# Performance work log

Measured on AMD Instinct MI355X. Metric: run time of the kernel, lower is better.

The kernel has to match this reference:

```python
import jax, jax.numpy as jnp
import numpy as np
from jax import lax

B, NPG, IN, OUT, ETYPES, STEPS, E = 16, 1024, 128, 256, 2, 6, 262144
N = B * NPG
CONCAT = IN + OUT
EPS = 1e-5


def setup_inputs() -> dict:
    key = jax.random.key(0)
    ks = jax.random.split(key, 24)
    s = 0.05
    return {
        "features": jax.random.normal(ks[0], (N, IN), jnp.float32),
        "src": jax.random.randint(ks[1], (E,), 0, N, jnp.int32),
        "dst": jax.random.randint(ks[2], (E,), 0, N, jnp.int32),
        "etype": jax.random.randint(ks[3], (E,), 0, ETYPES, jnp.int32),
        # GGNN per-etype linears (weight, bias) and GRUCell params
        "W_lin": jax.random.normal(ks[4], (ETYPES, OUT, OUT), jnp.float32) * s,
        "b_lin": jnp.zeros((ETYPES, OUT), jnp.float32),
        "W_ih": jax.random.normal(ks[5], (3 * OUT, OUT), jnp.float32) * s,
        "W_hh": jax.random.normal(ks[6], (3 * OUT, OUT), jnp.float32) * s,
        "b_ih": jnp.zeros((3 * OUT,), jnp.float32),
        "b_hh": jnp.zeros((3 * OUT,), jnp.float32),
        # conv branch on h_i (OUT channels)
        "conv1_w": jax.random.normal(ks[7], (OUT, OUT, 3), jnp.float32) * s,
        "conv1_b": jnp.zeros((OUT,), jnp.float32),
        "conv2_w": jax.random.normal(ks[8], (OUT, OUT, 1), jnp.float32) * s,
        "conv2_b": jnp.zeros((OUT,), jnp.float32),
        # conv branch on c_i (CONCAT channels)
        "convc1_w": jax.random.normal(ks[9], (CONCAT, CONCAT, 3), jnp.float32) * s,
        "convc1_b": jnp.zeros((CONCAT,), jnp.float32),
        "convc2_w": jax.random.normal(ks[10], (CONCAT, CONCAT, 1), jnp.float32) * s,
        "convc2_b": jnp.zeros((CONCAT,), jnp.float32),
        # shared batchnorms (training-mode batch stats, affine params)
        "bn_g": jnp.ones((OUT,), jnp.float32),
        "bn_b": jnp.zeros((OUT,), jnp.float32),
        "bnc_g": jnp.ones((CONCAT,), jnp.float32),
        "bnc_b": jnp.zeros((CONCAT,), jnp.float32),
        # gating MLPs
        "mlpy_w": jax.random.normal(ks[11], (2, OUT), jnp.float32) * s,
        "mlpy_b": jnp.zeros((2,), jnp.float32),
        "mlpz_w": jax.random.normal(ks[12], (2, CONCAT), jnp.float32) * s,
        "mlpz_b": jnp.zeros((2,), jnp.float32),
    }


def _bn_relu(x, g, b):  # x: [B, C, L], training-mode BN (biased var)
    mean = x.mean(axis=(0, 2), keepdims=True)
    var = ((x - mean) ** 2).mean(axis=(0, 2), keepdims=True)
    xn = (x - mean) * lax.rsqrt(var + EPS)
    return jax.nn.relu(xn * g[None, :, None] + b[None, :, None])


def _conv1d(x, w, b):  # x: [B, C, L], w: [O, I, K]
    y = lax.conv_general_dilated(x, w, (1,), 'VALID',
                                 dimension_numbers=('NCH', 'OIH', 'NCH'))
    return y + b[None, :, None]


def _maxpool(x, k, s):
    return lax.reduce_window(x, -jnp.inf, lax.max, (1, 1, k), (1, 1, s), 'VALID')


def _forward(features, src, dst, etype, W_lin, b_lin, W_ih, W_hh, b_ih, b_hh,
             conv1_w, conv1_b, conv2_w, conv2_b, convc1_w, convc1_b,
             convc2_w, convc2_b, bn_g, bn_b, bnc_g, bnc_b,
             mlpy_w, mlpy_b, mlpz_w, mlpz_b):
    # --- GatedGraphConv (DGL semantics): pad, n_steps of msg-pass + GRUCell ---
    h = jnp.pad(features, ((0, 0), (0, OUT - IN)))  # [N, OUT]
    for _ in range(STEPS):
        # per-etype linear applied to all nodes: [ETYPES, N, OUT]
        Wh = jnp.einsum('nd,ekd->enk', h, W_lin) + b_lin[:, None, :]
        msg = Wh[etype, src]                              # [E, OUT] gather
        agg = jax.ops.segment_sum(msg, dst, num_segments=N)  # scatter-add
        gi = agg @ W_ih.T + b_ih
        gh = h @ W_hh.T + b_hh
        ir, iz, ig = jnp.split(gi, 3, axis=-1)
        hr, hz, hg = jnp.split(gh, 3, axis=-1)
        r = jax.nn.sigmoid(ir + hr)
        z = jax.nn.sigmoid(iz + hz)
        n = jnp.tanh(ig + r * hg)
        h = (1.0 - z) * n + z * h

    h_i = h.reshape(B, NPG, OUT)
    x_i = features.reshape(B, NPG, IN)
    c_i = jnp.concatenate([h_i, x_i], axis=-1)  # [B, NPG, CONCAT]

    hT = jnp.swapaxes(h_i, 1, 2)  # [B, OUT, NPG]
    Y1 = _maxpool(_bn_relu(_conv1d(hT, conv1_w, conv1_b), bn_g, bn_b), 3, 2)
    Y2 = jnp.swapaxes(_maxpool(_bn_relu(_conv1d(Y1, conv2_w, conv2_b), bn_g, bn_b), 2, 2), 1, 2)

    cT = jnp.swapaxes(c_i, 1, 2)  # [B, CONCAT, NPG]
    Z1 = _maxpool(_bn_relu(_conv1d(cT, convc1_w, convc1_b), bnc_g, bnc_b), 3, 2)
    Z2 = jnp.swapaxes(_maxpool(_bn_relu(_conv1d(Z1, convc2_w, convc2_b), bnc_g, bnc_b), 2, 2), 1, 2)

    before_avg = (Y2 @ mlpy_w.T + mlpy_b) * (Z2 @ mlpz_w.T + mlpz_b)  # [B, L, 2]
    return jax.nn.sigmoid(before_avg.mean(axis=1))  # [B, 2]


def reference(features, src, dst, etype, W_lin, b_lin, W_ih, W_hh, b_ih, b_hh,
              conv1_w, conv1_b, conv2_w, conv2_b, convc1_w, convc1_b,
              convc2_w, convc2_b, bn_g, bn_b, bnc_g, bnc_b,
              mlpy_w, mlpy_b, mlpz_w, mlpz_b):
    return _forward(features, src, dst, etype, W_lin, b_lin, W_ih, W_hh, b_ih, b_hh,
                    conv1_w, conv1_b, conv2_w, conv2_b, convc1_w, convc1_b,
                    convc2_w, convc2_b, bn_g, bn_b, bnc_g, bnc_b,
                    mlpy_w, mlpy_b, mlpz_w, mlpz_b)
```

## Files before the change

kernel.cpp:

```cpp
#include <hip/hip_runtime.h>
#include <math.h>

constexpr int Bn     = 16;
constexpr int NPG    = 1024;
constexpr int Nn     = Bn * NPG;
constexpr int FIN    = 128;
constexpr int FOUT   = 256;
constexpr int CCAT   = 384;
constexpr int STEPS  = 6;
constexpr int NE     = 262144;

using short8 = __attribute__((ext_vector_type(8))) short;
using f32x4  = __attribute__((ext_vector_type(4))) float;

static __device__ __forceinline__ unsigned short f2bf(float x) {
    union { float f; unsigned u; } v; v.f = x;
    unsigned r = (v.u + 0x7FFFu + ((v.u >> 16) & 1u)) >> 16;
    return (unsigned short)r;
}
static __device__ __forceinline__ float bf2f(unsigned short b) {
    union { unsigned u; float f; } v; v.u = ((unsigned)b) << 16;
    return v.f;
}
static __device__ __forceinline__ float sigm(float x) { return 1.f / (1.f + expf(-x)); }

static __device__ __forceinline__ void gload16(const void* g, void* l) {
    __builtin_amdgcn_global_load_lds(
        (const __attribute__((address_space(1))) void*)g,
        (__attribute__((address_space(3))) void*)l, 16, 0, 0);
}


__global__ void cvt_bf(const float* __restrict__ s, unsigned short* __restrict__ d, int n) {
    int i = blockIdx.x * 256 + threadIdx.x;
    if (i < n) d[i] = f2bf(s[i]);
}

__global__ void cvt_wcat(const float* __restrict__ Wih, const float* __restrict__ Whh,
                         unsigned short* __restrict__ Wcat) {
    int o = blockIdx.x * 256 + threadIdx.x;
    int k = o >> 9, j = o & 511;
    float v = (j < 256) ? Whh[(size_t)k * 256 + j] : Wih[(size_t)k * 256 + (j - 256)];
    Wcat[o] = f2bf(v);
}

__global__ void add_bias(const float* __restrict__ a, const float* __restrict__ b,
                         float* __restrict__ o, int n) {
    int i = blockIdx.x * 256 + threadIdx.x;
    if (i < n) o[i] = a[i] + b[i];
}

__global__ void cvt_wconv(const float* __restrict__ W, unsigned short* __restrict__ Wt,
                          int C, int KW, int n) {
    int o = blockIdx.x * 256 + threadIdx.x;
    if (o >= n) return;
    int c = o / (KW * C), rem = o % (KW * C);
    int kb = rem / C, i = rem % C;
    Wt[o] = f2bf(W[(size_t)(c * C + i) * KW + kb]);
}

__global__ void pad_h(const float* __restrict__ f, float* __restrict__ h,
                      unsigned short* __restrict__ Acat) {
    int i = blockIdx.x * 256 + threadIdx.x;
    int k = i & 255, n = i >> 8;
    float v = (k < FIN) ? f[(size_t)n * FIN + k] : 0.f;
    h[i] = v; Acat[(size_t)n * 512 + k] = f2bf(v);
}

__global__ void build_cb(const unsigned short* __restrict__ Acat, const float* __restrict__ f,
                         unsigned short* __restrict__ cb) {
    int idx = blockIdx.x * 256 + threadIdx.x;
    int c = idx % CCAT, n = idx / CCAT;
    cb[idx] = (c < FOUT) ? Acat[(size_t)n * 512 + c] : f2bf(f[(size_t)n * FIN + (c - FOUT)]);
}


__global__ void edge_count(const int* __restrict__ dst, int* __restrict__ deg) {
    int e = blockIdx.x * 256 + threadIdx.x;
    atomicAdd(&deg[dst[e]], 1);
}

__global__ __launch_bounds__(1024) void scan_deg(const int* __restrict__ deg,
                                                 int* __restrict__ rowptr,
                                                 int* __restrict__ cursor) {
    __shared__ int ps[1024];
    const int t = threadIdx.x;
    int loc[16]; int s = 0;
    const int base = t * 16;
#pragma unroll
    for (int i = 0; i < 16; ++i) { loc[i] = deg[base + i]; s += loc[i]; }
    ps[t] = s;
    __syncthreads();
    for (int off = 1; off < 1024; off <<= 1) {
        int add = (t >= off) ? ps[t - off] : 0;
        __syncthreads();
        ps[t] += add;
        __syncthreads();
    }
    int run = ps[t] - s;
#pragma unroll
    for (int i = 0; i < 16; ++i) { rowptr[base + i] = run; cursor[base + i] = run; run += loc[i]; }
    if (t == 1023) rowptr[16384] = run;
}

__global__ void edge_fill(const int* __restrict__ src, const int* __restrict__ dst,
                          const int* __restrict__ et, int* __restrict__ cursor,
                          int* __restrict__ widx) {
    int e = blockIdx.x * 256 + threadIdx.x;
    int slot = atomicAdd(&cursor[dst[e]], 1);
    widx[slot] = src[e] * 2 + et[e];
}

static __device__ __forceinline__ void gemm128_body(
    const unsigned short* __restrict__ Ab, const unsigned short* __restrict__ W,
    const float* __restrict__ bias, float* __restrict__ Cf,
    unsigned short* __restrict__ Cb, int Ctap, int lda, int L, int Lv, int N, int K,
    int outBf, int l0, int col0, unsigned short* As, unsigned short* Bs) {
    const int t = threadIdx.x;
    const int w = t >> 6, l = t & 63;
    const int lr = l & 15, lhi = l >> 4;
    const int wr = w >> 1, wc = w & 1;
    const int srow8 = l >> 3;
    const int scole = ((l & 7) ^ srow8) * 8;
    const int lx7 = l & 7;

    f32x4 acc[4][4] = {};

    for (int k0 = 0; k0 < K; k0 += 64) {
        const int kb = k0 / Ctap;
        const int i0 = k0 - kb * Ctap;
        __syncthreads();
#pragma unroll
        for (int p = 0; p < 4; ++p) {
            const int r = w * 32 + p * 8;
            int srow = l0 + r + srow8 + kb;
            srow = srow < L ? srow : L - 1;
            gload16(Ab + (size_t)srow * lda + i0 + scole, &As[r * 64]);
            gload16(W + (size_t)(col0 + r + srow8) * K + k0 + scole, &Bs[r * 64]);
        }
        __syncthreads();
        const int abase = (wr * 64 + lr) * 64;
        const int bbase = (wc * 64 + lr) * 64;
#pragma unroll
        for (int kk = 0; kk < 2; ++kk) {
            const int soff = ((kk * 4 + lhi) ^ lx7) * 8;
            short8 af[4], bw[4];
#pragma unroll
            for (int fi = 0; fi < 4; ++fi)
                af[fi] = *(const short8*)&As[abase + fi * 1024 + soff];
#pragma unroll
            for (int fj = 0; fj < 4; ++fj)
                bw[fj] = *(const short8*)&Bs[bbase + fj * 1024 + soff];
#pragma unroll
            for (int fi = 0; fi < 4; ++fi)
#pragma unroll
                for (int fj = 0; fj < 4; ++fj)
                    acc[fi][fj] = __builtin_amdgcn_mfma_f32_16x16x32_bf16(
                        af[fi], bw[fj], acc[fi][fj], 0, 0, 0);
        }
    }
    const int rb = lhi * 4;
#pragma unroll
    for (int fi = 0; fi < 4; ++fi)
#pragma unroll
        for (int fj = 0; fj < 4; ++fj) {
            const int gcol = col0 + wc * 64 + fj * 16 + lr;
            const float bv = bias[gcol];
#pragma unroll
            for (int rr = 0; rr < 4; ++rr) {
                const int grow = l0 + wr * 64 + fi * 16 + rb + rr;
                if (grow < Lv) {
                    float v = acc[fi][fj][rr] + bv;
                    const size_t o = (size_t)grow * N + gcol;
                    if (outBf) Cb[o] = f2bf(v);
                    else       Cf[o] = v;
                }
            }
        }
}

__global__ __launch_bounds__(256) void gemm128_swz(
    const unsigned short* __restrict__ A, const unsigned short* __restrict__ W,
    const float* __restrict__ bias, unsigned short* __restrict__ Cb,
    int lda, int N, int K) {
    __shared__ unsigned short As[128 * 64];
    __shared__ unsigned short Bs[128 * 64];
    const int gX = gridDim.x;
    const int hId = blockIdx.x + gX * blockIdx.y;
    const int xcd = hId & 7, tt = hId >> 3;
    const int bx = tt % gX, by = xcd + 8 * (tt / gX);
    gemm128_body(A, W, bias, nullptr, Cb, lda, lda, Nn, Nn, N, K, 1,
                 by * 128, bx * 128, As, Bs);
}

__global__ __launch_bounds__(256) void gemm128_pair2(
    const unsigned short* __restrict__ A1, const unsigned short* __restrict__ W1,
    const float* __restrict__ b1, float* __restrict__ C1,
    int Ctap1, int lda1, int L1, int Lv1, int N1, int K1, int nx1, int ny1,
    const unsigned short* __restrict__ A2, const unsigned short* __restrict__ W2,
    const float* __restrict__ b2, float* __restrict__ C2,
    int Ctap2, int lda2, int L2, int Lv2, int N2, int K2, int nx2, int ny2) {
    __shared__ unsigned short As[128 * 64];
    __shared__ unsigned short Bs[128 * 64];
    int id = blockIdx.x;
    const int n1 = nx1 * ny1 * Bn;
    if (id < n1) {
        int x = id % nx1, y = (id / nx1) % ny1, z = id / (nx1 * ny1);
        gemm128_body(A1 + (size_t)z * L1 * lda1, W1, b1,
                     C1 + (size_t)z * Lv1 * N1, nullptr,
                     Ctap1, lda1, L1, Lv1, N1, K1, 0, y * 128, x * 128, As, Bs);
    } else {
        id -= n1;
        int x = id % nx2, y = (id / nx2) % ny2, z = id / (nx2 * ny2);
        gemm128_body(A2 + (size_t)z * L2 * lda2, W2, b2,
                     C2 + (size_t)z * Lv2 * N2, nullptr,
                     Ctap2, lda2, L2, Lv2, N2, K2, 0, y * 128, x * 128, As, Bs);
    }
}

__global__ __launch_bounds__(256) void gemm_gru(
    const unsigned short* __restrict__ Acat, const unsigned short* __restrict__ Wcat,
    const unsigned short* __restrict__ Whg, const float* __restrict__ bias_s,
    const float* __restrict__ bias_g, float* __restrict__ h,
    unsigned short* __restrict__ Anext) {
    __shared__ unsigned short As[64 * 64];
    __shared__ unsigned short Bs[256 * 64];
    const int hId = blockIdx.x + 4 * blockIdx.y;
    const int xcd = hId & 7, tt = hId >> 3;
    const int bx = tt & 3, by = xcd + 8 * (tt >> 2);
    const int l0 = by * 64, c0 = bx * 64;

    const int t = threadIdx.x;
    const int w = t >> 6, l = t & 63;
    const int lr = l & 15, lhi = l >> 4;
    const int srow8 = l >> 3;
    const int scole = ((l & 7) ^ srow8) * 8;
    const int lx7 = l & 7;

    f32x4 acc[16] = {};

#pragma unroll
    for (int k0 = 0; k0 < 512; k0 += 64) {
        __syncthreads();
#pragma unroll
        for (int p = 0; p < 2; ++p) {
            const int r = w * 16 + p * 8;
            gload16(Acat + (size_t)(l0 + r + srow8) * 512 + k0 + scole, &As[r * 64]);
        }
#pragma unroll
        for (int p = 0; p < 8; ++p) {
            const int r = w * 64 + p * 8;
            if (r < 192) {
                const int g = r >> 6;
                const int cr = (r & 63) + srow8;
                gload16(Wcat + (size_t)(g * 256 + c0 + cr) * 512 + k0 + scole, &Bs[r * 64]);
            } else if (k0 < 256) {
                const int cr = (r - 192) + srow8;
                gload16(Whg + (size_t)(c0 + cr) * 256 + k0 + scole, &Bs[r * 64]);
            }
        }
        __syncthreads();
        const int abase = (w * 16 + lr) * 64;
#pragma unroll
        for (int kk = 0; kk < 2; ++kk) {
            const int soff = ((kk * 4 + lhi) ^ lx7) * 8;
            short8 a0 = *(const short8*)&As[abase + soff];
#pragma unroll
            for (int g = 0; g < 4; ++g) {
                if (!(g == 3 && k0 >= 256)) {
#pragma unroll
                    for (int fj = 0; fj < 4; ++fj) {
                        short8 bb = *(const short8*)&Bs[(g * 64 + fj * 16 + lr) * 64 + soff];
                        acc[g * 4 + fj] = __builtin_amdgcn_mfma_f32_16x16x32_bf16(
                            a0, bb, acc[g * 4 + fj], 0, 0, 0);
                    }
                }
            }
        }
    }
    const int rb = lhi * 4;
#pragma unroll
    for (int fj = 0; fj < 4; ++fj) {
        const int c = c0 + fj * 16 + lr;
        const float br = bias_s[c];
        const float bz = bias_s[256 + c];
        const float bg = bias_s[512 + c];
        const float bh = bias_g[c];
#pragma unroll
        for (int rr = 0; rr < 4; ++rr) {
            const int grow = l0 + w * 16 + rb + rr;
            float sr = acc[0 * 4 + fj][rr] + br;
            float sz = acc[1 * 4 + fj][rr] + bz;
            float sg = acc[2 * 4 + fj][rr] + bg;
            float hg = acc[3 * 4 + fj][rr] + bh;
            float r = sigm(sr), z = sigm(sz);
            float nn = tanhf(sg - (1.f - r) * hg);
            const size_t ho = (size_t)grow * 256 + c;
            float hv = (1.f - z) * nn + z * h[ho];
            h[ho] = hv;
            Anext[(size_t)grow * 512 + c] = f2bf(hv);
        }
    }
}

__global__ __launch_bounds__(64) void gather_agg(
    const unsigned short* __restrict__ Whb, const int* __restrict__ rowptr,
    const int* __restrict__ widx, unsigned short* __restrict__ Acat) {
    const int n = blockIdx.x, t = threadIdx.x;
    const int s0 = rowptr[n], s1 = rowptr[n + 1];
    float p0[4] = {}, p1[4] = {}, p2[4] = {}, p3[4] = {};
    int s = s0;
    for (; s + 4 <= s1; s += 4) {
        const int w0 = widx[s], w1 = widx[s + 1], w2 = widx[s + 2], w3 = widx[s + 3];
        const ushort4 v0 = *(const ushort4*)(Whb + (size_t)w0 * 256 + t * 4);
        const ushort4 v1 = *(const ushort4*)(Whb + (size_t)w1 * 256 + t * 4);
        const ushort4 v2 = *(const ushort4*)(Whb + (size_t)w2 * 256 + t * 4);
        const ushort4 v3 = *(const ushort4*)(Whb + (size_t)w3 * 256 + t * 4);
        p0[0] += bf2f(v0.x); p0[1] += bf2f(v0.y); p0[2] += bf2f(v0.z); p0[3] += bf2f(v0.w);
        p1[0] += bf2f(v1.x); p1[1] += bf2f(v1.y); p1[2] += bf2f(v1.z); p1[3] += bf2f(v1.w);
        p2[0] += bf2f(v2.x); p2[1] += bf2f(v2.y); p2[2] += bf2f(v2.z); p2[3] += bf2f(v2.w);
        p3[0] += bf2f(v3.x); p3[1] += bf2f(v3.y); p3[2] += bf2f(v3.z); p3[3] += bf2f(v3.w);
    }
    for (; s < s1; ++s) {
        const int wi = widx[s];
        const ushort4 v = *(const ushort4*)(Whb + (size_t)wi * 256 + t * 4);
        p0[0] += bf2f(v.x); p0[1] += bf2f(v.y); p0[2] += bf2f(v.z); p0[3] += bf2f(v.w);
    }
    ushort4 o;
    o.x = f2bf(p0[0] + p1[0] + p2[0] + p3[0]);
    o.y = f2bf(p0[1] + p1[1] + p2[1] + p3[1]);
    o.z = f2bf(p0[2] + p1[2] + p2[2] + p3[2]);
    o.w = f2bf(p0[3] + p1[3] + p2[3] + p3[3]);
    *(ushort4*)(Acat + (size_t)n * 512 + 256 + t * 4) = o;
}

constexpr int NCHUNK = 128;

static __device__ __forceinline__ void bn_part_body(
    const float* __restrict__ X, float* __restrict__ pS, float* __restrict__ pQ,
    int C, int totalRows, int rowsPerChunk, int bx, int by) {
    const int t  = threadIdx.x;
    const int cq = t & 31, rl = t >> 5;
    const int c0 = bx * 128 + cq * 4;
    const int r0 = by * rowsPerChunk;
    const int r1 = min(r0 + rowsPerChunk, totalRows);
    float s0 = 0, s1 = 0, s2 = 0, s3 = 0, q0 = 0, q1 = 0, q2 = 0, q3 = 0;
    for (int r = r0 + rl; r < r1; r += 8) {
        float4 v = *(const float4*)(X + (size_t)r * C + c0);
        s0 += v.x; s1 += v.y; s2 += v.z; s3 += v.w;
        q0 += v.x * v.x; q1 += v.y * v.y; q2 += v.z * v.z; q3 += v.w * v.w;
    }
    __shared__ float ls[8][128], lq[8][128];
    ls[rl][cq * 4 + 0] = s0; ls[rl][cq * 4 + 1] = s1;
    ls[rl][cq * 4 + 2] = s2; ls[rl][cq * 4 + 3] = s3;
    lq[rl][cq * 4 + 0] = q0; lq[rl][cq * 4 + 1] = q1;
    lq[rl][cq * 4 + 2] = q2; lq[rl][cq * 4 + 3] = q3;
    __syncthreads();
    if (rl == 0) {
#pragma unroll
        for (int i = 0; i < 4; ++i) {
            const int c = cq * 4 + i;
            float ss = 0, qq = 0;
#pragma unroll
            for (int j = 0; j < 8; ++j) { ss += ls[j][c]; qq += lq[j][c]; }
            pS[(size_t)by * C + c0 + i] = ss;
            pQ[(size_t)by * C + c0 + i] = qq;
        }
    }
}

__global__ __launch_bounds__(256) void bn_part_pair(
    const float* __restrict__ X1, float* __restrict__ pS1, float* __restrict__ pQ1, int C1,
    const float* __restrict__ X2, float* __restrict__ pS2, float* __restrict__ pQ2, int C2,
    int totalRows, int rowsPerChunk) {
    int id = blockIdx.x;
    const int n1 = (C1 / 128) * NCHUNK;
    if (id < n1)
        bn_part_body(X1, pS1, pQ1, C1, totalRows, rowsPerChunk, id % (C1 / 128), id / (C1 / 128));
    else {
        id -= n1;
        bn_part_body(X2, pS2, pQ2, C2, totalRows, rowsPerChunk, id % (C2 / 128), id / (C2 / 128));
    }
}

__global__ __launch_bounds__(128) void bn_reduce_pair(
    const float* __restrict__ pS1, const float* __restrict__ pQ1,
    float* __restrict__ mean1, float* __restrict__ var1, int C1,
    const float* __restrict__ pS2, const float* __restrict__ pQ2,
    float* __restrict__ mean2, float* __restrict__ var2, int C2, int totalRows) {
    int c = blockIdx.x;
    const float* pS; const float* pQ; float* mean; float* var; int C;
    if (c < C1) { pS = pS1; pQ = pQ1; mean = mean1; var = var1; C = C1; }
    else { c -= C1; pS = pS2; pQ = pQ2; mean = mean2; var = var2; C = C2; }
    const int t = threadIdx.x;
    __shared__ float rs[128], rq[128];
    rs[t] = pS[(size_t)t * C + c];
    rq[t] = pQ[(size_t)t * C + c];
    __syncthreads();
    for (int st = 64; st; st >>= 1) {
        if (t < st) { rs[t] += rs[t + st]; rq[t] += rq[t + st]; }
        __syncthreads();
    }
    if (t == 0) {
        float m = rs[0] / totalRows;
        mean[c] = m;
        var[c]  = rq[0] / totalRows - m * m;
    }
}

static __device__ __forceinline__ void bnp_body(
    const float* __restrict__ X, const float* __restrict__ mean,
    const float* __restrict__ var, const float* __restrict__ g,
    const float* __restrict__ bta, float* __restrict__ Of,
    unsigned short* __restrict__ Ob, int C, int Lin, int Lout, int Kp, int outBf, int idx) {
    if (idx >= Bn * Lout * C) return;
    int c = idx % C, j = (idx / C) % Lout, b = idx / (C * Lout);
    float sc = g[c] * rsqrtf(var[c] + 1e-5f);
    float sh = bta[c] - mean[c] * sc;
    const float* xb = X + ((size_t)b * Lin + j * 2) * C + c;
    float m = 0.f;
    for (int k = 0; k < Kp; ++k) m = fmaxf(m, xb[(size_t)k * C] * sc + sh);
    if (outBf) Ob[idx] = f2bf(m);
    else       Of[idx] = m;
}

__global__ void bnp_pair(
    const float* __restrict__ X1, const float* __restrict__ mean1,
    const float* __restrict__ var1, const float* __restrict__ g1,
    const float* __restrict__ b1, float* __restrict__ Of1,
    unsigned short* __restrict__ Ob1, int C1,
    const float* __restrict__ X2, const float* __restrict__ mean2,
    const float* __restrict__ var2, const float* __restrict__ g2,
    const float* __restrict__ b2, float* __restrict__ Of2,
    unsigned short* __restrict__ Ob2, int C2,
    int Lin, int Lout, int Kp, int outBf) {
    int id = blockIdx.x;
    const int nb1 = (Bn * Lout * C1 + 255) / 256;
    if (id < nb1)
        bnp_body(X1, mean1, var1, g1, b1, Of1, Ob1, C1, Lin, Lout, Kp, outBf,
                 id * 256 + threadIdx.x);
    else
        bnp_body(X2, mean2, var2, g2, b2, Of2, Ob2, C2, Lin, Lout, Kp, outBf,
                 (id - nb1) * 256 + threadIdx.x);
}

__global__ void final_dot(const float* __restrict__ Y2, const float* __restrict__ Z2,
                          const float* __restrict__ wy, const float* __restrict__ by,
                          const float* __restrict__ wz, const float* __restrict__ bz,
                          float* __restrict__ prod) {
    const int b = blockIdx.y, j = blockIdx.x, t = threadIdx.x;
    float p0 = 0, p1 = 0, q0 = 0, q1 = 0;
    const float* yrow = Y2 + (size_t)(b * 255 + j) * FOUT;
    const float* zrow = Z2 + (size_t)(b * 255 + j) * CCAT;
    for (int c = t; c < FOUT; c += 128) {
        float v = yrow[c];
        p0 += v * wy[c]; p1 += v * wy[FOUT + c];
    }
    for (int c = t; c < CCAT; c += 128) {
        float v = zrow[c];
        q0 += v * wz[c]; q1 += v * wz[CCAT + c];
    }
    __shared__ float r0[128], r1[128], r2[128], r3[128];
    r0[t] = p0; r1[t] = p1; r2[t] = q0; r3[t] = q1;
    __syncthreads();
    for (int s = 64; s; s >>= 1) {
        if (t < s) { r0[t] += r0[t + s]; r1[t] += r1[t + s]; r2[t] += r2[t + s]; r3[t] += r3[t + s]; }
        __syncthreads();
    }
    if (t == 0) {
        float y0 = r0[0] + by[0], y1 = r1[0] + by[1];
        float z0 = r2[0] + bz[0], z1 = r3[0] + bz[1];
        prod[((size_t)b * 255 + j) * 2 + 0] = y0 * z0;
        prod[((size_t)b * 255 + j) * 2 + 1] = y1 * z1;
    }
}

__global__ void final_out(const float* __restrict__ prod, float* __restrict__ out) {
    const int b = blockIdx.x, t = threadIdx.x;
    const int w = t >> 6, lane = t & 63;
    float s = 0.f;
    for (int j = lane; j < 255; j += 64) s += prod[((size_t)b * 255 + j) * 2 + w];
#pragma unroll
    for (int off = 32; off; off >>= 1) s += __shfl_down(s, off);
    if (lane == 0) out[b * 2 + w] = 1.f / (1.f + expf(-s / 255.f));
}

extern "C" void kernel_launch(void* const* d_in, const int* in_sizes, int n_in,
                              void* d_out, int out_size, void* d_ws, size_t ws_size,
                              hipStream_t stream) {
    (void)in_sizes; (void)n_in; (void)out_size; (void)ws_size;
    const float* features = (const float*)d_in[0];
    const int*   src      = (const int*)d_in[1];
    const int*   dst      = (const int*)d_in[2];
    const int*   etype    = (const int*)d_in[3];
    const float* W_lin    = (const float*)d_in[4];
    const float* b_lin    = (const float*)d_in[5];
    const float* W_ih     = (const float*)d_in[6];
    const float* W_hh     = (const float*)d_in[7];
    const float* b_ih     = (const float*)d_in[8];
    const float* b_hh     = (const float*)d_in[9];
    const float* conv1_w  = (const float*)d_in[10];
    const float* conv1_b  = (const float*)d_in[11];
    const float* conv2_w  = (const float*)d_in[12];
    const float* conv2_b  = (const float*)d_in[13];
    const float* convc1_w = (const float*)d_in[14];
    const float* convc1_b = (const float*)d_in[15];
    const float* convc2_w = (const float*)d_in[16];
    const float* convc2_b = (const float*)d_in[17];
    const float* bn_g     = (const float*)d_in[18];
    const float* bn_b     = (const float*)d_in[19];
    const float* bnc_g    = (const float*)d_in[20];
    const float* bnc_b    = (const float*)d_in[21];
    const float* mlpy_w   = (const float*)d_in[22];
    const float* mlpy_b   = (const float*)d_in[23];
    const float* mlpz_w   = (const float*)d_in[24];
    const float* mlpz_b   = (const float*)d_in[25];

    float* ws = (float*)d_ws;
    float*          h      = ws;
    unsigned short* Acat0  = (unsigned short*)(ws + 4194304);
    float*          bufA   = ws + 8388608;
    float*          bufB   = ws + 20971520;
    unsigned short* Wlin_b = (unsigned short*)(ws + 33554432);
    unsigned short* Whh_b  = (unsigned short*)(ws + 33554432) + 131072;
    unsigned short* Wcat_b = (unsigned short*)(ws + 33554432) + 327680;
    float*          bias_s = ws + 33950000;
    int*            ib     = (int*)(ws + 34000000);
    int* deg    = ib;
    int* cursor = ib + 16384;
    int* rowptr = ib + 32768;
    int* widx   = ib + 49160;
    float* sreg = ws + 34500000;
    float* meanY = sreg;
    float* varY  = sreg + 256;
    float* meanZ = sreg + 512;
    float* varZ  = sreg + 896;
    float* pSy   = sreg + 1280;
    float* pQy   = sreg + 34048;
    float* pSz   = sreg + 66816;
    float* pQz   = sreg + 115968;
    float* prod  = sreg + 165120;

    unsigned short* Whb   = (unsigned short*)bufA;
    unsigned short* Acat1 = (unsigned short*)(bufA + 4194304);
    const unsigned short* Whg = Whh_b + 512 * 256;

    cvt_bf<<<512,  256, 0, stream>>>(W_lin, Wlin_b, 131072);
    cvt_bf<<<768,  256, 0, stream>>>(W_hh,  Whh_b,  196608);
    cvt_wcat<<<1536, 256, 0, stream>>>(W_ih, W_hh, Wcat_b);
    add_bias<<<3, 256, 0, stream>>>(b_ih, b_hh, bias_s, 768);
    pad_h<<<Nn * FOUT / 256, 256, 0, stream>>>(features, h, Acat0);

    hipMemsetAsync(deg, 0, 16384 * sizeof(int), stream);
    edge_count<<<NE / 256, 256, 0, stream>>>(dst, deg);
    scan_deg<<<1, 1024, 0, stream>>>(deg, rowptr, cursor);
    edge_fill<<<NE / 256, 256, 0, stream>>>(src, dst, etype, cursor, widx);

    unsigned short* Acur = Acat0;
    unsigned short* Anxt = Acat1;
    for (int s6 = 0; s6 < STEPS; ++s6) {
        gemm128_swz<<<dim3(4, 128), 256, 0, stream>>>(
            Acur, Wlin_b, b_lin, Whb, 512, 512, 256);
        gather_agg<<<Nn, 64, 0, stream>>>(Whb, rowptr, widx, Acur);
        gemm_gru<<<dim3(4, 256), 256, 0, stream>>>(
            Acur, Wcat_b, Whg, bias_s, b_hh + 512, h, Anxt);
        unsigned short* tmp = Acur; Acur = Anxt; Anxt = tmp;
    }

    unsigned short* cb    = (unsigned short*)ws;
    float*          Yc1   = bufA;
    unsigned short* P1y   = (unsigned short*)(bufA + 4186112);
    float*          Yc2   = bufA + 5230592;
    float*          Y2    = bufA + 7319552;
    float*          Z2    = bufA + 8364032;
    float*          Zc1   = bufB;
    unsigned short* P1z   = (unsigned short*)(bufB + 6279168);
    float*          Zc2   = bufB + 7845888;
    unsigned short* Wcv   = (unsigned short*)(bufB + 11000000);
    unsigned short* c1b   = Wcv;
    unsigned short* c2b   = Wcv + 196608;
    unsigned short* cc1b  = Wcv + 262144;
    unsigned short* cc2b  = Wcv + 704512;

    cvt_wconv<<<768,  256, 0, stream>>>(conv1_w,  c1b,  FOUT, 3, FOUT * FOUT * 3);
    cvt_wconv<<<256,  256, 0, stream>>>(conv2_w,  c2b,  FOUT, 1, FOUT * FOUT);
    cvt_wconv<<<1728, 256, 0, stream>>>(convc1_w, cc1b, CCAT, 3, CCAT * CCAT * 3);
    cvt_wconv<<<576,  256, 0, stream>>>(convc2_w, cc2b, CCAT, 1, CCAT * CCAT);
    build_cb<<<Nn * CCAT / 256, 256, 0, stream>>>(Acat0, features, cb);

    const int rows1 = Bn * 1022;
    const int rows2 = Bn * 510;
    const int rpc1  = (rows1 + NCHUNK - 1) / NCHUNK;
    const int rpc2  = (rows2 + NCHUNK - 1) / NCHUNK;

    gemm128_pair2<<<2 * 8 * Bn + 3 * 8 * Bn, 256, 0, stream>>>(
        Acat0, c1b, conv1_b, Yc1, FOUT, 512, 1024, 1022, FOUT, 768, 2, 8,
        cb, cc1b, convc1_b, Zc1, CCAT, 384, 1024, 1022, CCAT, 1152, 3, 8);
    bn_part_pair<<<(2 + 3) * NCHUNK, 256, 0, stream>>>(
        Yc1, pSy, pQy, FOUT, Zc1, pSz, pQz, CCAT, rows1, rpc1);
    bn_reduce_pair<<<FOUT + CCAT, 128, 0, stream>>>(
        pSy, pQy, meanY, varY, FOUT, pSz, pQz, meanZ, varZ, CCAT, rows1);
    {
        const int nb1 = (Bn * 510 * FOUT + 255) / 256;
        const int nb2 = (Bn * 510 * CCAT + 255) / 256;
        bnp_pair<<<nb1 + nb2, 256, 0, stream>>>(
            Yc1, meanY, varY, bn_g, bn_b, nullptr, P1y, FOUT,
            Zc1, meanZ, varZ, bnc_g, bnc_b, nullptr, P1z, CCAT, 1022, 510, 3, 1);
    }

    gemm128_pair2<<<2 * 4 * Bn + 3 * 4 * Bn, 256, 0, stream>>>(
        P1y, c2b, conv2_b, Yc2, FOUT, 256, 510, 510, FOUT, 256, 2, 4,
        P1z, cc2b, convc2_b, Zc2, CCAT, 384, 510, 510, CCAT, 384, 3, 4);
    bn_part_pair<<<(2 + 3) * NCHUNK, 256, 0, stream>>>(
        Yc2, pSy, pQy, FOUT, Zc2, pSz, pQz, CCAT, rows2, rpc2);
    bn_reduce_pair<<<FOUT + CCAT, 128, 0, stream>>>(
        pSy, pQy, meanY, varY, FOUT, pSz, pQz, meanZ, varZ, CCAT, rows2);
    {
        const int nb1 = (Bn * 255 * FOUT + 255) / 256;
        const int nb2 = (Bn * 255 * CCAT + 255) / 256;
        bnp_pair<<<nb1 + nb2, 256, 0, stream>>>(
            Yc2, meanY, varY, bn_g, bn_b, Y2, nullptr, FOUT,
            Zc2, meanZ, varZ, bnc_g, bnc_b, Z2, nullptr, CCAT, 510, 255, 2, 0);
    }

    final_dot<<<dim3(255, Bn), 128, 0, stream>>>(Y2, Z2, mlpy_w, mlpy_b, mlpz_w, mlpz_b, prod);
    final_out<<<Bn, 128, 0, stream>>>(prod, (float*)d_out);
}
```

Baseline: 609.0 us.

## Store conv outputs in bf16, remap pair GEMM blocks, pack gather nodes per block

The conv GEMM outputs (Yc1, Yc2, Zc1, Zc2) are now written as bf16 instead of fp32, and the batchnorm statistics and BN+maxpool kernels read bf16. This halves the memory traffic for those intermediates. The paired conv GEMM also remaps block IDs so that consecutive tiles are spread across the XCDs. The gather aggregation now runs four nodes per 256-thread block instead of one node per 64-thread block, which reduces the block count and scheduling overhead. The bf16 intermediates cost precision in the batchnorm statistics.

```diff
diff --git a/kernel.cpp b/kernel.cpp
--- a/kernel.cpp
+++ b/kernel.cpp
@@ -195,26 +195,27 @@
 
 __global__ __launch_bounds__(256) void gemm128_pair2(
     const unsigned short* __restrict__ A1, const unsigned short* __restrict__ W1,
-    const float* __restrict__ b1, float* __restrict__ C1,
+    const float* __restrict__ b1, unsigned short* __restrict__ C1,
     int Ctap1, int lda1, int L1, int Lv1, int N1, int K1, int nx1, int ny1,
     const unsigned short* __restrict__ A2, const unsigned short* __restrict__ W2,
-    const float* __restrict__ b2, float* __restrict__ C2,
+    const float* __restrict__ b2, unsigned short* __restrict__ C2,
     int Ctap2, int lda2, int L2, int Lv2, int N2, int K2, int nx2, int ny2) {
     __shared__ unsigned short As[128 * 64];
     __shared__ unsigned short Bs[128 * 64];
-    int id = blockIdx.x;
+    const int G = gridDim.x;
+    int id = (blockIdx.x & 7) * (G >> 3) + (blockIdx.x >> 3);
     const int n1 = nx1 * ny1 * Bn;
     if (id < n1) {
         int x = id % nx1, y = (id / nx1) % ny1, z = id / (nx1 * ny1);
-        gemm128_body(A1 + (size_t)z * L1 * lda1, W1, b1,
-                     C1 + (size_t)z * Lv1 * N1, nullptr,
-                     Ctap1, lda1, L1, Lv1, N1, K1, 0, y * 128, x * 128, As, Bs);
+        gemm128_body(A1 + (size_t)z * L1 * lda1, W1, b1, nullptr,
+                     C1 + (size_t)z * Lv1 * N1,
+                     Ctap1, lda1, L1, Lv1, N1, K1, 1, y * 128, x * 128, As, Bs);
     } else {
         id -= n1;
         int x = id % nx2, y = (id / nx2) % ny2, z = id / (nx2 * ny2);
-        gemm128_body(A2 + (size_t)z * L2 * lda2, W2, b2,
-                     C2 + (size_t)z * Lv2 * N2, nullptr,
-                     Ctap2, lda2, L2, Lv2, N2, K2, 0, y * 128, x * 128, As, Bs);
+        gemm128_body(A2 + (size_t)z * L2 * lda2, W2, b2, nullptr,
+                     C2 + (size_t)z * Lv2 * N2,
+                     Ctap2, lda2, L2, Lv2, N2, K2, 1, y * 128, x * 128, As, Bs);
     }
 }
 
@@ -303,10 +304,11 @@
     }
 }
 
-__global__ __launch_bounds__(64) void gather_agg(
+__global__ __launch_bounds__(256) void gather_agg(
     const unsigned short* __restrict__ Whb, const int* __restrict__ rowptr,
     const int* __restrict__ widx, unsigned short* __restrict__ Acat) {
-    const int n = blockIdx.x, t = threadIdx.x;
+    const int n = blockIdx.x * 4 + (threadIdx.x >> 6);
+    const int t = threadIdx.x & 63;
     const int s0 = rowptr[n], s1 = rowptr[n + 1];
     float p0[4] = {}, p1[4] = {}, p2[4] = {}, p3[4] = {};
     int s = s0;
@@ -337,7 +339,7 @@
 constexpr int NCHUNK = 128;
 
 static __device__ __forceinline__ void bn_part_body(
-    const float* __restrict__ X, float* __restrict__ pS, float* __restrict__ pQ,
+    const unsigned short* __restrict__ X, float* __restrict__ pS, float* __restrict__ pQ,
     int C, int totalRows, int rowsPerChunk, int bx, int by) {
     const int t  = threadIdx.x;
     const int cq = t & 31, rl = t >> 5;
@@ -346,9 +348,10 @@
     const int r1 = min(r0 + rowsPerChunk, totalRows);
     float s0 = 0, s1 = 0, s2 = 0, s3 = 0, q0 = 0, q1 = 0, q2 = 0, q3 = 0;
     for (int r = r0 + rl; r < r1; r += 8) {
-        float4 v = *(const float4*)(X + (size_t)r * C + c0);
-        s0 += v.x; s1 += v.y; s2 += v.z; s3 += v.w;
-        q0 += v.x * v.x; q1 += v.y * v.y; q2 += v.z * v.z; q3 += v.w * v.w;
+        ushort4 u = *(const ushort4*)(X + (size_t)r * C + c0);
+        float v0 = bf2f(u.x), v1 = bf2f(u.y), v2 = bf2f(u.z), v3 = bf2f(u.w);
+        s0 += v0; s1 += v1; s2 += v2; s3 += v3;
+        q0 += v0 * v0; q1 += v1 * v1; q2 += v2 * v2; q3 += v3 * v3;
     }
     __shared__ float ls[8][128], lq[8][128];
     ls[rl][cq * 4 + 0] = s0; ls[rl][cq * 4 + 1] = s1;
@@ -370,8 +373,8 @@
 }
 
 __global__ __launch_bounds__(256) void bn_part_pair(
-    const float* __restrict__ X1, float* __restrict__ pS1, float* __restrict__ pQ1, int C1,
-    const float* __restrict__ X2, float* __restrict__ pS2, float* __restrict__ pQ2, int C2,
+    const unsigned short* __restrict__ X1, float* __restrict__ pS1, float* __restrict__ pQ1, int C1,
+    const unsigned short* __restrict__ X2, float* __restrict__ pS2, float* __restrict__ pQ2, int C2,
     int totalRows, int rowsPerChunk) {
     int id = blockIdx.x;
     const int n1 = (C1 / 128) * NCHUNK;
@@ -409,7 +412,7 @@
 }
 
 static __device__ __forceinline__ void bnp_body(
-    const float* __restrict__ X, const float* __restrict__ mean,
+    const unsigned short* __restrict__ X, const float* __restrict__ mean,
     const float* __restrict__ var, const float* __restrict__ g,
     const float* __restrict__ bta, float* __restrict__ Of,
     unsigned short* __restrict__ Ob, int C, int Lin, int Lout, int Kp, int outBf, int idx) {
@@ -417,19 +420,19 @@
     int c = idx % C, j = (idx / C) % Lout, b = idx / (C * Lout);
     float sc = g[c] * rsqrtf(var[c] + 1e-5f);
     float sh = bta[c] - mean[c] * sc;
-    const float* xb = X + ((size_t)b * Lin + j * 2) * C + c;
+    const unsigned short* xb = X + ((size_t)b * Lin + j * 2) * C + c;
     float m = 0.f;
-    for (int k = 0; k < Kp; ++k) m = fmaxf(m, xb[(size_t)k * C] * sc + sh);
+    for (int k = 0; k < Kp; ++k) m = fmaxf(m, bf2f(xb[(size_t)k * C]) * sc + sh);
     if (outBf) Ob[idx] = f2bf(m);
     else       Of[idx] = m;
 }
 
 __global__ void bnp_pair(
-    const float* __restrict__ X1, const float* __restrict__ mean1,
+    const unsigned short* __restrict__ X1, const float* __restrict__ mean1,
     const float* __restrict__ var1, const float* __restrict__ g1,
     const float* __restrict__ b1, float* __restrict__ Of1,
     unsigned short* __restrict__ Ob1, int C1,
-    const float* __restrict__ X2, const float* __restrict__ mean2,
+    const unsigned short* __restrict__ X2, const float* __restrict__ mean2,
     const float* __restrict__ var2, const float* __restrict__ g2,
     const float* __restrict__ b2, float* __restrict__ Of2,
     unsigned short* __restrict__ Ob2, int C2,
@@ -561,21 +564,21 @@
     for (int s6 = 0; s6 < STEPS; ++s6) {
         gemm128_swz<<<dim3(4, 128), 256, 0, stream>>>(
             Acur, Wlin_b, b_lin, Whb, 512, 512, 256);
-        gather_agg<<<Nn, 64, 0, stream>>>(Whb, rowptr, widx, Acur);
+        gather_agg<<<Nn / 4, 256, 0, stream>>>(Whb, rowptr, widx, Acur);
         gemm_gru<<<dim3(4, 256), 256, 0, stream>>>(
             Acur, Wcat_b, Whg, bias_s, b_hh + 512, h, Anxt);
         unsigned short* tmp = Acur; Acur = Anxt; Anxt = tmp;
     }
 
     unsigned short* cb    = (unsigned short*)ws;
-    float*          Yc1   = bufA;
+    unsigned short* Yc1   = (unsigned short*)bufA;
     unsigned short* P1y   = (unsigned short*)(bufA + 4186112);
-    float*          Yc2   = bufA + 5230592;
+    unsigned short* Yc2   = (unsigned short*)(bufA + 5230592);
     float*          Y2    = bufA + 7319552;
     float*          Z2    = bufA + 8364032;
-    float*          Zc1   = bufB;
+    unsigned short* Zc1   = (unsigned short*)bufB;
     unsigned short* P1z   = (unsigned short*)(bufB + 6279168);
-    float*          Zc2   = bufB + 7845888;
+    unsigned short* Zc2   = (unsigned short*)(bufB + 7845888);
     unsigned short* Wcv   = (unsigned short*)(bufB + 11000000);
     unsigned short* c1b   = Wcv;
     unsigned short* c2b   = Wcv + 196608;
```

Measured after the change: 611.7 us, median of 3. About the same (+0.5%).
